# Optimization experiments

Hardware: AMD Instinct MI355X
Metric: run time of the kernel (lower is better)

Reference implementation:

```python
import jax, jax.numpy as jnp
import numpy as np

COMMITMENT_LOSS_WEIGHT = 0.25


def setup_inputs() -> dict:
    key = jax.random.key(0)
    k1, k2 = jax.random.split(key)
    B, H, W, C = 64, 32, 32, 256
    D, K = H * W, 1024  # embedding_dim = H*W per the rearrange+reshape in call()
    x = jax.random.normal(k1, (B, H, W, C), dtype=jnp.float32)
    # Orthogonal initializer (like tf.keras.initializers.Orthogonal) via QR
    E = jnp.linalg.qr(jax.random.normal(k2, (D, K), dtype=jnp.float32))[0]
    return {"x": x, "embeddings": E.astype(jnp.float32)}


def reference(x, embeddings):
    B, H, W, C = x.shape
    D = H * W  # embedding_dim
    # einops: 'b h w c -> b c (h w)'
    cont = jnp.transpose(x, (0, 3, 1, 2)).reshape(B, C, D)
    flat = cont.reshape(-1, D)  # [B*C, D]
    # squared L2 distances via norm + matmul (as in get_discretised)
    dists = (jnp.sum(flat * flat, axis=1, keepdims=True)
             + jnp.sum(embeddings * embeddings, axis=0)
             - 2.0 * (flat @ embeddings))  # [B*C, K]
    idx = jnp.argmin(dists, axis=1)  # [B*C]
    # one_hot @ embeddings.T == direct gather of codebook columns
    quantised = embeddings.T[idx].reshape(B, C, D)
    codebook_loss = jnp.mean((jax.lax.stop_gradient(cont) - quantised) ** 2)
    commitment_loss = COMMITMENT_LOSS_WEIGHT * jnp.mean(
        (cont - jax.lax.stop_gradient(quantised)) ** 2)
    loss = codebook_loss + commitment_loss  # layer add_loss terms, summed
    # einops: 'b c (h w) -> b h w c'
    q_bhwc = jnp.transpose(quantised.reshape(B, C, H, W), (0, 2, 3, 1))
    discretised = idx.reshape(-1, C)  # [B, C]
    # straight-through estimator
    q_out = x + jax.lax.stop_gradient(q_bhwc - x)
    return q_out, discretised, loss
```

## Files before the change

kernel.cpp:

```cpp
#include <hip/hip_runtime.h>
#include <float.h>
#include <stdint.h>

#define B_   64
#define C_   256
#define D_   1024
#define K_   1024
#define M_   16384
#define NX_  16777216
#define DISC_OFF NX_
#define LOSS_OFF (NX_ + M_)

typedef _Float16 h8 __attribute__((ext_vector_type(8)));
typedef float    f4 __attribute__((ext_vector_type(4)));

#define XSCALE 512.0f
#define ESCALE 2048.0f
#define DOT_UNSCALE_2 (2.0f / 1048576.0f)

#define WS_EH  0
#define WS_EL  524288
#define WS_CN  1048576
#define WS_PCN 1049600
#define WS_PV  1049600
#define WS_PI  1180672

__device__ __forceinline__ void async16(const _Float16* g, _Float16* l) {
    __builtin_amdgcn_global_load_lds(
        (const __attribute__((address_space(1))) unsigned int*)g,
        (__attribute__((address_space(3))) unsigned int*)l, 16, 0, 0);
}

__global__ __launch_bounds__(256) void split_kernel(const float* __restrict__ x,
                                                    const float* __restrict__ E,
                                                    _Float16* __restrict__ Xh,
                                                    _Float16* __restrict__ Xl,
                                                    _Float16* __restrict__ Eh,
                                                    _Float16* __restrict__ El,
                                                    float* __restrict__ pcn) {
    const int bid = blockIdx.x;
    if (bid < 512) {
        const int tid = bid * 256 + threadIdx.x;
        const int n   = tid & 1023;
        const int o   = tid >> 10;
        const int d0  = o * 8;
        h8 hh, ll;
        float s = 0.f;
        #pragma unroll
        for (int i = 0; i < 8; ++i) {
            const float v = E[(size_t)(d0 + i) * K_ + n];
            s = fmaf(v, v, s);
            const float vs = v * ESCALE;
            const _Float16 h = (_Float16)vs;
            hh[i] = h;
            ll[i] = (_Float16)(vs - (float)h);
        }
        pcn[o * K_ + n] = s;
        const int nt   = n >> 4;
        const int kt   = o >> 2;
        const int lane = (n & 15) + (o & 3) * 16;
        const size_t off = ((size_t)(nt * 32 + kt) * 64 + lane) * 8;
        *(h8*)(Eh + off) = hh;
        *(h8*)(El + off) = ll;
    } else {
        const int tid = (bid - 512) * 256 + threadIdx.x;
        const int m   = tid & 16383;
        const int o   = tid >> 14;
        const int b   = m >> 8, c = m & 255;
        const int d0  = o * 8;
        const float* xp = x + ((size_t)(b * 1024 + d0) * 256) + c;
        h8 hh, ll;
        #pragma unroll
        for (int i = 0; i < 8; ++i) {
            const float v  = xp[(size_t)i * 256];
            const float vs = v * XSCALE;
            const _Float16 h = (_Float16)vs;
            hh[i] = h;
            ll[i] = (_Float16)(vs - (float)h);
        }
        const int mt   = m >> 4;
        const int kt   = o >> 2;
        const int lane = (m & 15) + (o & 3) * 16;
        const size_t off = ((size_t)(mt * 32 + kt) * 64 + lane) * 8;
        *(h8*)(Xh + off) = hh;
        *(h8*)(Xl + off) = ll;
    }
}

__global__ __launch_bounds__(256) void colnorm2_kernel(const float* __restrict__ pcn,
                                                       float* __restrict__ cn,
                                                       float* __restrict__ loss_slot) {
    __shared__ float sp[4][64];
    const int t    = threadIdx.x;
    const int col  = blockIdx.x * 64 + (t & 63);
    const int part = t >> 6;
    float s = 0.f;
    #pragma unroll 8
    for (int i = 0; i < 32; ++i) s += pcn[(part * 32 + i) * K_ + col];
    sp[part][t & 63] = s;
    __syncthreads();
    if (t < 64) cn[col] = (sp[0][t] + sp[1][t]) + (sp[2][t] + sp[3][t]);
    if (blockIdx.x == 0 && t == 0) *loss_slot = 0.0f;
}

__global__ __launch_bounds__(512, 4) void gemm_argmin_kernel(
        const _Float16* __restrict__ Xh, const _Float16* __restrict__ Xl,
        const _Float16* __restrict__ Eh, const _Float16* __restrict__ El,
        const float* __restrict__ cn,
        float* __restrict__ pV, int* __restrict__ pI) {
    extern __shared__ _Float16 smem[];
    _Float16* Ab0 = smem;
    _Float16* Ab1 = smem + 8192;
    _Float16* Bb0 = smem + 16384;
    _Float16* Bb1 = smem + 24576;
    float* cV = (float*)(smem + 32768);
    int*   cI = (int*)(cV + 512);

    const int t    = threadIdx.x;
    const int bid  = blockIdx.x;
    const int swz  = (bid & 7) * 128 + (bid >> 3);
    const int rt   = swz >> 3;
    const int ct   = swz & 7;
    const int wave = t >> 6, lane = t & 63;
    const int lo16 = lane & 15, hi4 = lane >> 4;
    const int mq   = (wave & 1) * 64;
    const int nq   = (wave >> 1) * 32;
    const int mt0  = rt * 8, nt0 = ct * 8;
    const int n0g  = ct * 128;

    const _Float16* src[4];
    _Float16* dst0[4];
    _Float16* dst1[4];
    #pragma unroll
    for (int i = 0; i < 4; ++i) {
        const int id = wave * 4 + i;
        if (id < 16) {
            const int plane = id >> 3, mt = id & 7;
            src[i]  = (plane ? Xl : Xh) + ((size_t)(mt0 + mt) * 32) * 512 + lane * 8;
            dst0[i] = Ab0 + (plane * 8 + mt) * 512 + lane * 8;
            dst1[i] = Ab1 + (plane * 8 + mt) * 512 + lane * 8;
        } else {
            const int q = id - 16;
            const int plane = q >> 3, nt = q & 7;
            src[i]  = (plane ? El : Eh) + ((size_t)(nt0 + nt) * 32) * 512 + lane * 8;
            dst0[i] = Bb0 + (plane * 8 + nt) * 512 + lane * 8;
            dst1[i] = Bb1 + (plane * 8 + nt) * 512 + lane * 8;
        }
    }

    f4 acc[4][2];
    const f4 zero = {0.f, 0.f, 0.f, 0.f};
    #pragma unroll
    for (int i = 0; i < 4; ++i)
        #pragma unroll
        for (int j = 0; j < 2; ++j) acc[i][j] = zero;

    #pragma unroll
    for (int i = 0; i < 4; ++i) async16(src[i], dst0[i]);

    for (int s = 0; s < 32; ++s) {
        const int cur = s & 1;
        __syncthreads();
        if (s + 1 < 32) {
            #pragma unroll
            for (int i = 0; i < 4; ++i)
                async16(src[i] + (size_t)(s + 1) * 512, cur ? dst0[i] : dst1[i]);
        }
        const _Float16* Abuf = cur ? Ab1 : Ab0;
        const _Float16* Bbuf = cur ? Bb1 : Bb0;

        h8 Bf[2][2];
        #pragma unroll
        for (int tn = 0; tn < 2; ++tn) {
            const int tixn = (nq >> 4) + tn;
            Bf[0][tn] = *(const h8*)&Bbuf[tixn * 512 + lane * 8];
            Bf[1][tn] = *(const h8*)&Bbuf[(8 + tixn) * 512 + lane * 8];
        }
        #pragma unroll
        for (int tm = 0; tm < 4; ++tm) {
            const int tixm = (mq >> 4) + tm;
            const h8 Ah = *(const h8*)&Abuf[tixm * 512 + lane * 8];
            const h8 Al = *(const h8*)&Abuf[(8 + tixm) * 512 + lane * 8];
            #pragma unroll
            for (int tn = 0; tn < 2; ++tn) {
                acc[tm][tn] = __builtin_amdgcn_mfma_f32_16x16x32_f16(Ah, Bf[0][tn], acc[tm][tn], 0, 0, 0);
                acc[tm][tn] = __builtin_amdgcn_mfma_f32_16x16x32_f16(Ah, Bf[1][tn], acc[tm][tn], 0, 0, 0);
                acc[tm][tn] = __builtin_amdgcn_mfma_f32_16x16x32_f16(Al, Bf[0][tn], acc[tm][tn], 0, 0, 0);
            }
        }
    }

    float cnv[2];
    #pragma unroll
    for (int tn = 0; tn < 2; ++tn) cnv[tn] = cn[n0g + nq + tn * 16 + lo16];

    #pragma unroll
    for (int tm = 0; tm < 4; ++tm) {
        #pragma unroll
        for (int r = 0; r < 4; ++r) {
            float bv = FLT_MAX;
            int   bi = 0;
            #pragma unroll
            for (int tn = 0; tn < 2; ++tn) {
                const float v = cnv[tn] - acc[tm][tn][r] * DOT_UNSCALE_2;
                if (v < bv) { bv = v; bi = nq + tn * 16 + lo16; }
            }
            #pragma unroll
            for (int msk = 1; msk < 16; msk <<= 1) {
                const float ov = __shfl_xor(bv, msk, 64);
                const int   oi = __shfl_xor(bi, msk, 64);
                if (ov < bv || (ov == bv && oi < bi)) { bv = ov; bi = oi; }
            }
            if (lo16 == 0) {
                const int row = mq + tm * 16 + hi4 * 4 + r;
                const int g   = wave >> 1;
                cV[row * 4 + g] = bv;
                cI[row * 4 + g] = bi;
            }
        }
    }
    __syncthreads();
    if (t < 128) {
        float bv = FLT_MAX;
        int   bi = 0;
        #pragma unroll
        for (int g = 0; g < 4; ++g) {
            const float v = cV[t * 4 + g];
            const int   i = cI[t * 4 + g];
            if (v < bv || (v == bv && i < bi)) { bv = v; bi = i; }
        }
        const int row = rt * 128 + t;
        pV[row * 8 + ct] = bv;
        pI[row * 8 + ct] = n0g + bi;
    }
}

__global__ __launch_bounds__(256) void reduce_kernel(const float* __restrict__ pV,
                                                     const int* __restrict__ pI,
                                                     float* __restrict__ disc) {
    const int rid = blockIdx.x * 256 + threadIdx.x;
    float bv = FLT_MAX;
    int   bi = 0;
    #pragma unroll
    for (int c = 0; c < 8; ++c) {
        const float v = pV[rid * 8 + c];
        const int   i = pI[rid * 8 + c];
        if (v < bv || (v == bv && i < bi)) { bv = v; bi = i; }
    }
    disc[rid] = (float)bi;
}

__global__ __launch_bounds__(256) void finalize_kernel(const float* __restrict__ x,
                                                       const float* __restrict__ E,
                                                       const float* __restrict__ discf,
                                                       float* __restrict__ out,
                                                       float* __restrict__ loss) {
    __shared__ float Erow[1024];
    const int t = threadIdx.x;
    const int d = blockIdx.x;
    *(float4*)&Erow[t * 4] = *(const float4*)(E + (size_t)d * K_ + t * 4);
    __syncthreads();

    const int bl = t >> 6;
    const int c4 = (t & 63) * 4;
    float lsum = 0.f;
    #pragma unroll 4
    for (int bg = 0; bg < 64; bg += 4) {
        const int b = bg + bl;
        const float4 id4 = *(const float4*)(discf + b * 256 + c4);
        const size_t xoff = ((size_t)(b * 1024 + d) << 8) + c4;
        const float4 xv = *(const float4*)(x + xoff);
        const float e0 = Erow[(int)id4.x];
        const float e1 = Erow[(int)id4.y];
        const float e2 = Erow[(int)id4.z];
        const float e3 = Erow[(int)id4.w];
        float4 qv;
        qv.x = xv.x + (e0 - xv.x);
        qv.y = xv.y + (e1 - xv.y);
        qv.z = xv.z + (e2 - xv.z);
        qv.w = xv.w + (e3 - xv.w);
        *(float4*)(out + xoff) = qv;
        const float d0 = xv.x - e0, d1 = xv.y - e1, d2 = xv.z - e2, d3 = xv.w - e3;
        lsum += fmaf(d0, d0, fmaf(d1, d1, fmaf(d2, d2, d3 * d3)));
    }

    #pragma unroll
    for (int off = 32; off > 0; off >>= 1)
        lsum += __shfl_down(lsum, off);
    __shared__ float wsum[4];
    if ((t & 63) == 0) wsum[t >> 6] = lsum;
    __syncthreads();
    if (t == 0) {
        const float s = (wsum[0] + wsum[1]) + (wsum[2] + wsum[3]);
        atomicAdd(loss, s * (1.25f / 16777216.0f));
    }
}

extern "C" void kernel_launch(void* const* d_in, const int* in_sizes, int n_in,
                              void* d_out, int out_size, void* d_ws, size_t ws_size,
                              hipStream_t stream) {
    (void)in_sizes; (void)n_in; (void)out_size; (void)ws_size;
    const float* x = (const float*)d_in[0];
    const float* E = (const float*)d_in[1];
    float* out = (float*)d_out;
    float* ws  = (float*)d_ws;

    _Float16* Eh = (_Float16*)(ws + WS_EH);
    _Float16* El = (_Float16*)(ws + WS_EL);
    float* cn    = ws + WS_CN;
    float* pcn   = ws + WS_PCN;
    float* pV    = ws + WS_PV;
    int*   pI    = (int*)(ws + WS_PI);

    _Float16* Xh = (_Float16*)out;
    _Float16* Xl = (_Float16*)out + NX_;
    float* disc  = out + DISC_OFF;
    float* loss  = out + LOSS_OFF;

    hipFuncSetAttribute((const void*)gemm_argmin_kernel,
                        hipFuncAttributeMaxDynamicSharedMemorySize, 69632);

    split_kernel   <<<8704, 256, 0, stream>>>(x, E, Xh, Xl, Eh, El, pcn);
    colnorm2_kernel<<<16,   256, 0, stream>>>(pcn, cn, loss);
    gemm_argmin_kernel<<<1024, 512, 69632, stream>>>(Xh, Xl, Eh, El, cn, pV, pI);
    reduce_kernel  <<<64,   256, 0, stream>>>(pV, pI, disc);
    finalize_kernel<<<1024, 256, 0, stream>>>(x, E, disc, out, loss);
}
```

Before: 254.1 us.

## Enlarge GEMM tile to 256x256 with 4-stage pipeline over split-precision passes

Each GEMM-argmin block now covers a 256x256 output tile instead of 128x128. The three hi/lo fp16 products become separate K-passes over one 4-buffer async staging ring with explicit vmcnt waits, raw barriers and raised MFMA priority. The aim is more MFMA work per LDS byte and fewer redundant global reads, by loading one plane pair per stage instead of both. In exchange it uses 128KB of LDS and many more accumulator registers, which lowers occupancy to 2 blocks per CU and leaves only 256 blocks. The partial-argmin reduction is resized to 4 column tiles to match.

```diff
diff --git a/kernel.cpp b/kernel.cpp
--- a/kernel.cpp
+++ b/kernel.cpp
@@ -103,107 +103,106 @@
     if (blockIdx.x == 0 && t == 0) *loss_slot = 0.0f;
 }
 
-__global__ __launch_bounds__(512, 4) void gemm_argmin_kernel(
+__global__ __launch_bounds__(512, 2) void gemm_argmin_kernel(
         const _Float16* __restrict__ Xh, const _Float16* __restrict__ Xl,
         const _Float16* __restrict__ Eh, const _Float16* __restrict__ El,
         const float* __restrict__ cn,
         float* __restrict__ pV, int* __restrict__ pI) {
     extern __shared__ _Float16 smem[];
-    _Float16* Ab0 = smem;
-    _Float16* Ab1 = smem + 8192;
-    _Float16* Bb0 = smem + 16384;
-    _Float16* Bb1 = smem + 24576;
-    float* cV = (float*)(smem + 32768);
-    int*   cI = (int*)(cV + 512);
-
     const int t    = threadIdx.x;
     const int bid  = blockIdx.x;
-    const int swz  = (bid & 7) * 128 + (bid >> 3);
-    const int rt   = swz >> 3;
-    const int ct   = swz & 7;
+    const int swz  = (bid & 7) * 32 + (bid >> 3);
+    const int rt   = swz >> 2;
+    const int ct   = swz & 3;
     const int wave = t >> 6, lane = t & 63;
     const int lo16 = lane & 15, hi4 = lane >> 4;
-    const int mq   = (wave & 1) * 64;
-    const int nq   = (wave >> 1) * 32;
-    const int mt0  = rt * 8, nt0 = ct * 8;
-    const int n0g  = ct * 128;
-
-    const _Float16* src[4];
-    _Float16* dst0[4];
-    _Float16* dst1[4];
+    const int wr   = wave & 1, wc = wave >> 1;
+    const int wr8  = wr * 8,  wc4 = wc * 4;
+    const int mt0  = rt * 16, nt0 = ct * 16;
+    const int n0g  = ct * 256;
+
+    size_t gOff[4]; int lOff[4]; bool aFlag[4];
     #pragma unroll
     for (int i = 0; i < 4; ++i) {
         const int id = wave * 4 + i;
         if (id < 16) {
-            const int plane = id >> 3, mt = id & 7;
-            src[i]  = (plane ? Xl : Xh) + ((size_t)(mt0 + mt) * 32) * 512 + lane * 8;
-            dst0[i] = Ab0 + (plane * 8 + mt) * 512 + lane * 8;
-            dst1[i] = Ab1 + (plane * 8 + mt) * 512 + lane * 8;
+            aFlag[i] = true;
+            gOff[i]  = (size_t)(mt0 + id) * 16384 + lane * 8;
+            lOff[i]  = id * 512 + lane * 8;
         } else {
-            const int q = id - 16;
-            const int plane = q >> 3, nt = q & 7;
-            src[i]  = (plane ? El : Eh) + ((size_t)(nt0 + nt) * 32) * 512 + lane * 8;
-            dst0[i] = Bb0 + (plane * 8 + nt) * 512 + lane * 8;
-            dst1[i] = Bb1 + (plane * 8 + nt) * 512 + lane * 8;
-        }
-    }
-
-    f4 acc[4][2];
+            aFlag[i] = false;
+            gOff[i]  = (size_t)(nt0 + (id - 16)) * 16384 + lane * 8;
+            lOff[i]  = 8192 + (id - 16) * 512 + lane * 8;
+        }
+    }
+
+    f4 acc[8][4];
     const f4 zero = {0.f, 0.f, 0.f, 0.f};
     #pragma unroll
-    for (int i = 0; i < 4; ++i)
-        #pragma unroll
-        for (int j = 0; j < 2; ++j) acc[i][j] = zero;
-
-    #pragma unroll
-    for (int i = 0; i < 4; ++i) async16(src[i], dst0[i]);
-
-    for (int s = 0; s < 32; ++s) {
-        const int cur = s & 1;
-        __syncthreads();
-        if (s + 1 < 32) {
+    for (int m = 0; m < 8; ++m)
+        #pragma unroll
+        for (int n = 0; n < 4; ++n) acc[m][n] = zero;
+
+    auto stage = [&](int s2) {
+        const int p  = s2 >> 5;
+        const int kk = s2 & 31;
+        const _Float16* Ab = (p < 2) ? Xh : Xl;
+        const _Float16* Bb = (p == 1) ? El : Eh;
+        _Float16* db = smem + (s2 & 3) * 16384;
+        #pragma unroll
+        for (int i = 0; i < 4; ++i)
+            async16((aFlag[i] ? Ab : Bb) + gOff[i] + (size_t)kk * 512, db + lOff[i]);
+    };
+
+    auto body = [&](int s, bool doStage) {
+        __builtin_amdgcn_s_barrier();
+        asm volatile("" ::: "memory");
+        if (doStage) stage(s + 3);
+        const _Float16* rb = smem + (s & 3) * 16384;
+        h8 Bf[4];
+        #pragma unroll
+        for (int n = 0; n < 4; ++n)
+            Bf[n] = *(const h8*)(rb + 8192 + (wc4 + n) * 512 + lane * 8);
+        __builtin_amdgcn_s_setprio(1);
+        #pragma unroll
+        for (int m = 0; m < 8; ++m) {
+            const h8 Af = *(const h8*)(rb + (wr8 + m) * 512 + lane * 8);
             #pragma unroll
-            for (int i = 0; i < 4; ++i)
-                async16(src[i] + (size_t)(s + 1) * 512, cur ? dst0[i] : dst1[i]);
-        }
-        const _Float16* Abuf = cur ? Ab1 : Ab0;
-        const _Float16* Bbuf = cur ? Bb1 : Bb0;
-
-        h8 Bf[2][2];
-        #pragma unroll
-        for (int tn = 0; tn < 2; ++tn) {
-            const int tixn = (nq >> 4) + tn;
-            Bf[0][tn] = *(const h8*)&Bbuf[tixn * 512 + lane * 8];
-            Bf[1][tn] = *(const h8*)&Bbuf[(8 + tixn) * 512 + lane * 8];
-        }
-        #pragma unroll
-        for (int tm = 0; tm < 4; ++tm) {
-            const int tixm = (mq >> 4) + tm;
-            const h8 Ah = *(const h8*)&Abuf[tixm * 512 + lane * 8];
-            const h8 Al = *(const h8*)&Abuf[(8 + tixm) * 512 + lane * 8];
-            #pragma unroll
-            for (int tn = 0; tn < 2; ++tn) {
-                acc[tm][tn] = __builtin_amdgcn_mfma_f32_16x16x32_f16(Ah, Bf[0][tn], acc[tm][tn], 0, 0, 0);
-                acc[tm][tn] = __builtin_amdgcn_mfma_f32_16x16x32_f16(Ah, Bf[1][tn], acc[tm][tn], 0, 0, 0);
-                acc[tm][tn] = __builtin_amdgcn_mfma_f32_16x16x32_f16(Al, Bf[0][tn], acc[tm][tn], 0, 0, 0);
-            }
-        }
-    }
-
-    float cnv[2];
-    #pragma unroll
-    for (int tn = 0; tn < 2; ++tn) cnv[tn] = cn[n0g + nq + tn * 16 + lo16];
-
-    #pragma unroll
-    for (int tm = 0; tm < 4; ++tm) {
+            for (int n = 0; n < 4; ++n)
+                acc[m][n] = __builtin_amdgcn_mfma_f32_16x16x32_f16(Af, Bf[n], acc[m][n], 0, 0, 0);
+        }
+        __builtin_amdgcn_s_setprio(0);
+    };
+
+    stage(0); stage(1); stage(2);
+
+    for (int s = 0; s < 94; ++s) {
+        asm volatile("s_waitcnt vmcnt(8)" ::: "memory");
+        body(s, s < 93);
+    }
+    asm volatile("s_waitcnt vmcnt(4)" ::: "memory");
+    body(94, false);
+    asm volatile("s_waitcnt vmcnt(0)" ::: "memory");
+    body(95, false);
+
+    __syncthreads();
+    float* cV = (float*)smem;
+    int*   cI = (int*)(cV + 1024);
+
+    float cnv[4];
+    #pragma unroll
+    for (int n = 0; n < 4; ++n) cnv[n] = cn[n0g + wc * 64 + n * 16 + lo16];
+
+    #pragma unroll
+    for (int m = 0; m < 8; ++m) {
         #pragma unroll
         for (int r = 0; r < 4; ++r) {
             float bv = FLT_MAX;
             int   bi = 0;
             #pragma unroll
-            for (int tn = 0; tn < 2; ++tn) {
-                const float v = cnv[tn] - acc[tm][tn][r] * DOT_UNSCALE_2;
-                if (v < bv) { bv = v; bi = nq + tn * 16 + lo16; }
+            for (int n = 0; n < 4; ++n) {
+                const float v = cnv[n] - acc[m][n][r] * DOT_UNSCALE_2;
+                if (v < bv) { bv = v; bi = wc * 64 + n * 16 + lo16; }
             }
             #pragma unroll
             for (int msk = 1; msk < 16; msk <<= 1) {
@@ -212,15 +211,14 @@
                 if (ov < bv || (ov == bv && oi < bi)) { bv = ov; bi = oi; }
             }
             if (lo16 == 0) {
-                const int row = mq + tm * 16 + hi4 * 4 + r;
-                const int g   = wave >> 1;
-                cV[row * 4 + g] = bv;
-                cI[row * 4 + g] = bi;
+                const int row = wr * 128 + m * 16 + hi4 * 4 + r;
+                cV[row * 4 + wc] = bv;
+                cI[row * 4 + wc] = bi;
             }
         }
     }
     __syncthreads();
-    if (t < 128) {
+    if (t < 256) {
         float bv = FLT_MAX;
         int   bi = 0;
         #pragma unroll
@@ -229,9 +227,9 @@
             const int   i = cI[t * 4 + g];
             if (v < bv || (v == bv && i < bi)) { bv = v; bi = i; }
         }
-        const int row = rt * 128 + t;
-        pV[row * 8 + ct] = bv;
-        pI[row * 8 + ct] = n0g + bi;
+        const int row = rt * 256 + t;
+        pV[row * 4 + ct] = bv;
+        pI[row * 4 + ct] = n0g + bi;
     }
 }
 
@@ -242,9 +240,9 @@
     float bv = FLT_MAX;
     int   bi = 0;
     #pragma unroll
-    for (int c = 0; c < 8; ++c) {
-        const float v = pV[rid * 8 + c];
-        const int   i = pI[rid * 8 + c];
+    for (int c = 0; c < 4; ++c) {
+        const float v = pV[rid * 4 + c];
+        const int   i = pI[rid * 4 + c];
         if (v < bv || (v == bv && i < bi)) { bv = v; bi = i; }
     }
     disc[rid] = (float)bi;
@@ -318,11 +316,11 @@
     float* loss  = out + LOSS_OFF;
 
     hipFuncSetAttribute((const void*)gemm_argmin_kernel,
-                        hipFuncAttributeMaxDynamicSharedMemorySize, 69632);
+                        hipFuncAttributeMaxDynamicSharedMemorySize, 131072);
 
     split_kernel   <<<8704, 256, 0, stream>>>(x, E, Xh, Xl, Eh, El, pcn);
     colnorm2_kernel<<<16,   256, 0, stream>>>(pcn, cn, loss);
-    gemm_argmin_kernel<<<1024, 512, 69632, stream>>>(Xh, Xl, Eh, El, cn, pV, pI);
+    gemm_argmin_kernel<<<256, 512, 131072, stream>>>(Xh, Xl, Eh, El, cn, pV, pI);
     reduce_kernel  <<<64,   256, 0, stream>>>(pV, pI, disc);
     finalize_kernel<<<1024, 256, 0, stream>>>(x, E, disc, out, loss);
 }
```

Result: no change. 253.9 us (-0.1%).
